# Kernel tuning notes

Hardware: AMD Instinct MI355X
Metric: run time of the kernel (lower is better)

The kernel has to match this reference:

```python
import jax, jax.numpy as jnp
import numpy as np

B, T, L, D = 2, 32, 64, 1024
H, WS, SH = 16, 8, 4
HD = D // H
EPS = 1e-6


def setup_inputs() -> dict:
    key = jax.random.key(0)
    ks = jax.random.split(key, 12)
    f = lambda i, shape, s=1.0: jax.random.normal(ks[i], shape, dtype=jnp.float32) * s
    return {
        'audio': f(0, (B, T, L, D)),
        'video': f(1, (B, T, L, D)),
        'image': f(2, (B, T, L, D)),
        'Wq': f(3, (3, D, D), 0.02), 'Wk': f(4, (3, D, D), 0.02),
        'Wv': f(5, (3, D, D), 0.02), 'Wp': f(6, (3, D, D), 0.02),
        'bq': jnp.zeros((3, D)), 'bk': jnp.zeros((3, D)),
        'bv': jnp.zeros((3, D)), 'bp': jnp.zeros((3, D)),
        'qn': jnp.ones((3, HD)), 'kn': jnp.ones((3, HD)),
        'rpb': f(7, (3, 2 * WS - 1, H), 0.02),
        'Wg1': f(8, (3 * D, 2 * D), 0.02), 'bg1': jnp.zeros((2 * D,)),
        'Wg2': f(9, (2 * D, 3), 0.02), 'bg2': jnp.zeros((3,)),
    }


def _rms(x, w):
    # OmniRMSNorm over last dim (head_dim)
    v = jnp.mean(x * x, axis=-1, keepdims=True)
    return w * (x * jax.lax.rsqrt(v + EPS))


def _wca(q_in, kv_in, Wq, bq, Wk, bk, Wv, bv, qn, kn, rpb, Wp, bp):
    """Shifted temporal-window cross attention. q_in, kv_in: [B,T,L,D]."""
    nw = T // WS
    S = WS * L  # tokens per window
    qr = jnp.roll(q_in, -SH, axis=1).reshape(B * nw, S, D)
    kr = jnp.roll(kv_in, -SH, axis=1).reshape(B * nw, S, D)
    q = (qr @ Wq + bq).reshape(B * nw, S, H, HD).transpose(0, 2, 1, 3)
    k = (kr @ Wk + bk).reshape(B * nw, S, H, HD).transpose(0, 2, 1, 3)
    v = (kr @ Wv + bv).reshape(B * nw, S, H, HD).transpose(0, 2, 1, 3)
    q = _rms(q, qn)
    k = _rms(k, kn)
    attn = jnp.einsum('bhqd,bhkd->bhqk', q, k) * (HD ** -0.5)
    # relative position bias over temporal coords within window: [H, WS, WS]
    coords = jnp.arange(WS)
    idx = coords[:, None] - coords[None, :] + WS - 1
    bias = rpb[idx].transpose(2, 0, 1)
    attn = attn.reshape(B * nw, H, WS, L, WS, L) + bias[None, :, :, None, :, None]
    attn = jax.nn.softmax(attn.reshape(B * nw, H, S, S), axis=-1)
    out = jnp.einsum('bhqk,bhkd->bhqd', attn, v)
    out = out.transpose(0, 2, 1, 3).reshape(B * nw, S, D) @ Wp + bp
    out = out.reshape(B, T, L, D)
    return jnp.roll(out, SH, axis=1)


def reference(audio, video, image, Wq, Wk, Wv, Wp, bq, bk, bv, bp,
              qn, kn, rpb, Wg1, bg1, Wg2, bg2):
    pairs = [(audio, video), (video, audio), (image, video)]
    feats = []
    for j, (qm, cm) in enumerate(pairs):
        o = _wca(qm, cm, Wq[j], bq[j], Wk[j], bk[j], Wv[j], bv[j],
                 qn[j], kn[j], rpb[j], Wp[j], bp[j])
        feats.append((qm + o).reshape(B, T * L, D))
    cat = jnp.concatenate(feats, axis=-1)                 # [B, TL, 3D]
    g = jax.nn.gelu(cat @ Wg1 + bg1, approximate=False) @ Wg2 + bg2
    gates = jax.nn.softmax(g, axis=-1)                    # [B, TL, 3]
    fused = sum(gates[..., m:m + 1] * feats[m] for m in range(3))
    return fused.reshape(B, T, L, D)
```

## Files before the change

### kernel.cpp

```cpp
#include <hip/hip_runtime.h>
#include <hip/hip_bf16.h>
#include <math.h>


typedef __bf16 bf16x8 __attribute__((ext_vector_type(8)));
typedef float f32x4 __attribute__((ext_vector_type(4)));

#define ELEM4M 4194304ull
#define ELEM1M 1048576ull

__device__ __forceinline__ float b2f(short s) {
    unsigned u = ((unsigned)(unsigned short)s) << 16;
    float f; __builtin_memcpy(&f, &u, 4); return f;
}
__device__ __forceinline__ short f2b(float f) {
    unsigned u; __builtin_memcpy(&u, &f, 4);
    u = (u + 0x7fffu + ((u >> 16) & 1u)) >> 16;
    return (short)u;
}

__global__ __launch_bounds__(256) void cast_roll_k(
    const float* __restrict__ a, const float* __restrict__ v,
    const float* __restrict__ im, short* __restrict__ dst)
{
    int z = blockIdx.y;
    const float* src = (z == 0) ? a : ((z == 1) ? v : im);
    int i = (blockIdx.x * 256 + threadIdx.x) * 4;
    int row = i >> 10, d = i & 1023;
    int b = row >> 11, tp = (row >> 6) & 31, l = row & 63;
    int srow = (b << 11) + (((tp + 4) & 31) << 6) + l;
    float4 val = *(const float4*)(src + (size_t)srow * 1024 + d);
    short4 o;
    o.x = f2b(val.x); o.y = f2b(val.y); o.z = f2b(val.z); o.w = f2b(val.w);
    *(short4*)(dst + (size_t)z * ELEM4M + i) = o;
}

__device__ __forceinline__ void transpose_body(const float* __restrict__ src,
                                               short* __restrict__ dst, int K, int N)
{
    __shared__ float tile[32][33];
    int x = blockIdx.x * 32 + threadIdx.x;
    int y0 = blockIdx.y * 32;
#pragma unroll
    for (int i = 0; i < 32; i += 8)
        tile[threadIdx.y + i][threadIdx.x] = src[(size_t)(y0 + threadIdx.y + i) * N + x];
    __syncthreads();
    int x2 = y0 + threadIdx.x;
    int y2 = blockIdx.x * 32 + threadIdx.y;
#pragma unroll
    for (int i = 0; i < 32; i += 8)
        dst[(size_t)(y2 + i) * K + x2] = f2b(tile[threadIdx.x][threadIdx.y + i]);
}

__global__ void transpose_qkvp_k(const float* Wq, const float* Wk, const float* Wv,
                                 const float* Wp, short* dst)
{
    int z = blockIdx.z;
    int g = z / 3, j = z - g * 3;
    const float* s4[4] = {Wq, Wk, Wv, Wp};
    transpose_body(s4[g] + (size_t)j * ELEM1M, dst + (size_t)z * ELEM1M, 1024, 1024);
}

__global__ void transpose_wg1_k(const float* Wg1, short* dst)
{
    transpose_body(Wg1, dst, 3072, 2048);
}

__global__ __launch_bounds__(256) void transpose_v_k(const short* __restrict__ V,
                                                     short* __restrict__ Vt)
{
    __shared__ short tile[64][65];
    int j = blockIdx.z;
    int c0 = blockIdx.x * 64, t0 = blockIdx.y * 64;
    const short* src = V + (size_t)j * ELEM4M;
    short* dst = Vt + (size_t)j * ELEM4M;
    int x = threadIdx.x & 63, y4 = threadIdx.x >> 6;
#pragma unroll
    for (int i = 0; i < 16; i++) {
        int row = y4 * 16 + i;
        tile[row][x] = src[(size_t)(t0 + row) * 1024 + c0 + x];
    }
    __syncthreads();
#pragma unroll
    for (int i = 0; i < 16; i++) {
        int row = y4 * 16 + i;
        dst[(size_t)(c0 + row) * 4096 + t0 + x] = tile[x][row];
    }
}

template<bool GELU, bool RES>
__device__ __forceinline__ void gemm_core(
    const short* __restrict__ A, const short* __restrict__ Wt,
    const float* __restrict__ bias, const short* __restrict__ Res,
    const float* __restrict__ nw, float nscale,
    short* __restrict__ C, int ldc, int colOff, int Ksz)
{
    __shared__ __align__(16) short As[128 * 32];
    __shared__ __align__(16) short Bs[128 * 32];
    const int tid = threadIdx.x;
    const int wave = tid >> 6, lane = tid & 63, quad = lane >> 4, l15 = lane & 15;
    const int wm = (wave & 1) * 64, wn = (wave >> 1) * 64;
    const int row0 = blockIdx.x * 128, col0 = blockIdx.y * 128;
    const int crow = lane >> 2, cseg = lane & 3;

    auto* As3 = (__attribute__((address_space(3))) short*)As;
    auto* Bs3 = (__attribute__((address_space(3))) short*)Bs;

    f32x4 acc[4][4];
#pragma unroll
    for (int i = 0; i < 4; i++)
#pragma unroll
        for (int jj = 0; jj < 4; jj++) acc[i][jj] = f32x4{0.f, 0.f, 0.f, 0.f};

    for (int k0 = 0; k0 < Ksz; k0 += 32) {
#pragma unroll
        for (int half = 0; half < 2; half++) {
            int chunk = wave + half * 4;
            const short* ga = A + (size_t)(row0 + chunk * 16 + crow) * Ksz + k0 + cseg * 8;
            const short* gb = Wt + (size_t)(col0 + chunk * 16 + crow) * Ksz + k0 + cseg * 8;
            __builtin_amdgcn_global_load_lds(
                (const __attribute__((address_space(1))) void*)ga,
                (__attribute__((address_space(3))) void*)(As3 + chunk * 512), 16, 0, 0);
            __builtin_amdgcn_global_load_lds(
                (const __attribute__((address_space(1))) void*)gb,
                (__attribute__((address_space(3))) void*)(Bs3 + chunk * 512), 16, 0, 0);
        }
        __syncthreads();
        bf16x8 af[4], bfr[4];
#pragma unroll
        for (int mi = 0; mi < 4; mi++)
            af[mi] = *(const bf16x8*)(As + (wm + mi * 16 + l15) * 32 + quad * 8);
#pragma unroll
        for (int ni = 0; ni < 4; ni++)
            bfr[ni] = *(const bf16x8*)(Bs + (wn + ni * 16 + l15) * 32 + quad * 8);
#pragma unroll
        for (int mi = 0; mi < 4; mi++)
#pragma unroll
            for (int ni = 0; ni < 4; ni++)
                acc[mi][ni] = __builtin_amdgcn_mfma_f32_16x16x32_bf16(
                    af[mi], bfr[ni], acc[mi][ni], 0, 0, 0);
        __syncthreads();
    }

    float bv4[4];
#pragma unroll
    for (int ni = 0; ni < 4; ni++) bv4[ni] = bias[col0 + wn + ni * 16 + l15];

    if (nw != nullptr) {
        float w4[4];
#pragma unroll
        for (int ni = 0; ni < 4; ni++) w4[ni] = nw[ni * 16 + l15];
#pragma unroll
        for (int mi = 0; mi < 4; mi++)
#pragma unroll
            for (int r = 0; r < 4; r++) {
                float v0 = acc[mi][0][r] + bv4[0];
                float v1 = acc[mi][1][r] + bv4[1];
                float v2 = acc[mi][2][r] + bv4[2];
                float v3 = acc[mi][3][r] + bv4[3];
                float ss = v0 * v0 + v1 * v1 + v2 * v2 + v3 * v3;
                ss += __shfl_xor(ss, 1); ss += __shfl_xor(ss, 2);
                ss += __shfl_xor(ss, 4); ss += __shfl_xor(ss, 8);
                float sc = rsqrtf(ss * (1.0f / 64.0f) + 1e-6f) * nscale;
                int row = row0 + wm + mi * 16 + quad * 4 + r;
                short* cp = C + (size_t)row * ldc + colOff + col0 + wn + l15;
                cp[0]  = f2b(v0 * sc * w4[0]);
                cp[16] = f2b(v1 * sc * w4[1]);
                cp[32] = f2b(v2 * sc * w4[2]);
                cp[48] = f2b(v3 * sc * w4[3]);
            }
    } else {
#pragma unroll
        for (int mi = 0; mi < 4; mi++)
#pragma unroll
            for (int ni = 0; ni < 4; ni++) {
                int col = col0 + wn + ni * 16 + l15;
#pragma unroll
                for (int r = 0; r < 4; r++) {
                    int row = row0 + wm + mi * 16 + quad * 4 + r;
                    float v = acc[mi][ni][r] + bv4[ni];
                    if (GELU) v = 0.5f * v * (1.0f + erff(v * 0.70710678118f));
                    if (RES)  v += b2f(Res[(size_t)row * 1024 + col]);
                    C[(size_t)row * ldc + colOff + col] = f2b(v);
                }
            }
    }
}

__global__ __launch_bounds__(256) void gemm_qkv_k(
    const short* r0, const short* r1, const short* r2,
    const short* Wt, const float* bq, const float* bk, const float* bv,
    const float* qn, const float* kn, short* qkv)
{
    int z = blockIdx.z;
    int g = z / 3, j = z - g * 3;
    const short* rolled[3] = {r0, r1, r2};
    const int kvmap[3] = {1, 0, 1};
    const short* A = (g == 0) ? rolled[j] : rolled[kvmap[j]];
    const float* bias = ((g == 0) ? bq : ((g == 1) ? bk : bv)) + j * 1024;
    const float* nw = (g == 0) ? (qn + j * 64) : ((g == 1) ? (kn + j * 64) : nullptr);
    float nscale = (g == 0) ? 0.125f : 1.0f;
    gemm_core<false, false>(A, Wt + (size_t)z * ELEM1M, bias, nullptr, nw, nscale,
                            qkv + (size_t)z * ELEM4M, 1024, 0, 1024);
}

__global__ __launch_bounds__(256) void gemm_out_k(
    const short* attnO, const short* Wt9, const float* bp,
    const short* r0, const short* r1, const short* r2, short* fcat)
{
    int j = blockIdx.z;
    const short* rolled[3] = {r0, r1, r2};
    gemm_core<false, true>(attnO + (size_t)j * ELEM4M, Wt9 + (size_t)j * ELEM1M,
                           bp + j * 1024, rolled[j], nullptr, 1.0f, fcat, 3072, j * 1024, 1024);
}

__global__ __launch_bounds__(256) void gemm_gate_k(
    const short* fcat, const short* Wg1t, const float* bg1, short* g1)
{
    gemm_core<true, false>(fcat, Wg1t, bg1, nullptr, nullptr, 1.0f, g1, 2048, 0, 3072);
}

__global__ __launch_bounds__(256, 2) void attn_k(
    const short* __restrict__ qkv, const short* __restrict__ Vt,
    const float* __restrict__ rpb, short* __restrict__ attnO)
{
    const int qhalf = blockIdx.x;
    const int win = blockIdx.y >> 4, h = blockIdx.y & 15;
    const int j = blockIdx.z;
    const int tid = threadIdx.x, wave = tid >> 6, lane = tid & 63;
    const int quad = lane >> 4, l15 = lane & 15;

    __shared__ __align__(16) short Ks[64 * 64];
    __shared__ __align__(16) short Vc[64 * 64];
    __shared__ __align__(16) short Ps[4][2][16 * 80];

    auto* Ks3 = (__attribute__((address_space(3))) short*)Ks;
    auto* Vc3 = (__attribute__((address_space(3))) short*)Vc;

    const int tq = qhalf * 4 + wave;
    const int qrow0 = win * 512 + tq * 64;
    const short* Qb = qkv + (size_t)j * ELEM4M + (size_t)qrow0 * 1024 + h * 64;
    const short* Kb = qkv + (size_t)(3 + j) * ELEM4M + (size_t)(win * 512) * 1024 + h * 64;
    const short* Vb = Vt + (size_t)j * ELEM4M + (size_t)(h * 64) * 4096 + win * 512;

    auto stage = [&](int ck) {
#pragma unroll
        for (int i = 0; i < 2; i++) {
            int s0 = (wave * 2 + i) * 64;
            int slot = s0 + lane;
            int r = slot >> 3, sw = ((slot & 7) ^ (r & 7)) * 8;
            const short* gk = Kb + (size_t)(ck * 64 + r) * 1024 + sw;
            const short* gv = Vb + (size_t)r * 4096 + ck * 64 + sw;
            __builtin_amdgcn_global_load_lds(
                (const __attribute__((address_space(1))) void*)gk,
                (__attribute__((address_space(3))) void*)(Ks3 + s0 * 8), 16, 0, 0);
            __builtin_amdgcn_global_load_lds(
                (const __attribute__((address_space(1))) void*)gv,
                (__attribute__((address_space(3))) void*)(Vc3 + s0 * 8), 16, 0, 0);
        }
    };

    bf16x8 qa[4][2];
#pragma unroll
    for (int qt = 0; qt < 4; qt++)
#pragma unroll
        for (int ks = 0; ks < 2; ks++)
            qa[qt][ks] = *(const bf16x8*)(Qb + (size_t)(qt * 16 + l15) * 1024
                                          + ks * 32 + quad * 8);

    f32x4 oacc[4][4];
#pragma unroll
    for (int qt = 0; qt < 4; qt++)
#pragma unroll
        for (int on = 0; on < 4; on++) oacc[qt][on] = f32x4{0.f, 0.f, 0.f, 0.f};
    float psum[4] = {0.f, 0.f, 0.f, 0.f};
    const float* rpbj = rpb + j * 240;

    stage(0);
    for (int ck = 0; ck < 8; ck++) {
        __syncthreads();
        bf16x8 kb[4][2], vb[4][2];
        const int swz = (l15 & 7);
#pragma unroll
        for (int t = 0; t < 4; t++)
#pragma unroll
            for (int ks = 0; ks < 2; ks++) {
                int row = t * 16 + l15;
                int off = row * 64 + (((ks * 4 + quad) ^ swz) * 8);
                kb[t][ks] = *(const bf16x8*)(Ks + off);
                vb[t][ks] = *(const bf16x8*)(Vc + off);
            }
        __syncthreads();
        if (ck < 7) stage(ck + 1);

        float bv = rpbj[(tq - ck + 7) * 16 + h];
#pragma unroll
        for (int qt = 0; qt < 4; qt++) {
            f32x4 sacc[4];
#pragma unroll
            for (int kn = 0; kn < 4; kn++) sacc[kn] = f32x4{0.f, 0.f, 0.f, 0.f};
#pragma unroll
            for (int ks = 0; ks < 2; ks++)
#pragma unroll
                for (int kn = 0; kn < 4; kn++)
                    sacc[kn] = __builtin_amdgcn_mfma_f32_16x16x32_bf16(
                        kb[kn][ks], qa[qt][ks], sacc[kn], 0, 0, 0);

            short* Pw = &Ps[wave][qt & 1][0];
            float ps = 0.f;
#pragma unroll
            for (int kn = 0; kn < 4; kn++) {
                float p0 = __expf(sacc[kn][0] + bv);
                float p1 = __expf(sacc[kn][1] + bv);
                float p2 = __expf(sacc[kn][2] + bv);
                float p3 = __expf(sacc[kn][3] + bv);
                ps += (p0 + p1) + (p2 + p3);
                short4 pk;
                pk.x = f2b(p0); pk.y = f2b(p1); pk.z = f2b(p2); pk.w = f2b(p3);
                *(short4*)(Pw + l15 * 80 + kn * 16 + quad * 4) = pk;
            }
            psum[qt] += ps;
#pragma unroll
            for (int ks = 0; ks < 2; ks++) {
                bf16x8 pa = *(const bf16x8*)(Pw + l15 * 80 + ks * 32 + quad * 8);
#pragma unroll
                for (int on = 0; on < 4; on++)
                    oacc[qt][on] = __builtin_amdgcn_mfma_f32_16x16x32_bf16(
                        pa, vb[on][ks], oacc[qt][on], 0, 0, 0);
            }
        }
    }

    short* Op = attnO + (size_t)j * ELEM4M;
#pragma unroll
    for (int qt = 0; qt < 4; qt++) {
        float s = psum[qt];
        s += __shfl_xor(s, 16); s += __shfl_xor(s, 32);
        float inv = 1.0f / s;
        float invr[4];
#pragma unroll
        for (int r = 0; r < 4; r++) invr[r] = __shfl(inv, quad * 4 + r);
#pragma unroll
        for (int on = 0; on < 4; on++) {
            int col = h * 64 + on * 16 + l15;
#pragma unroll
            for (int r = 0; r < 4; r++) {
                int row = qrow0 + qt * 16 + quad * 4 + r;
                Op[(size_t)row * 1024 + col] = f2b(oacc[qt][on][r] * invr[r]);
            }
        }
    }
}

__global__ __launch_bounds__(256) void fuse_k(
    const short* __restrict__ g1, const short* __restrict__ fcat,
    const float* __restrict__ Wg2, const float* __restrict__ bg2,
    float* __restrict__ out)
{
    int row = blockIdx.x, tid = threadIdx.x;
    const short* gp = g1 + (size_t)row * 2048;
    float a0 = 0.f, a1 = 0.f, a2 = 0.f;
    for (int k = tid; k < 2048; k += 256) {
        float gv = b2f(gp[k]);
        a0 += gv * Wg2[k * 3 + 0];
        a1 += gv * Wg2[k * 3 + 1];
        a2 += gv * Wg2[k * 3 + 2];
    }
#pragma unroll
    for (int off = 1; off < 64; off <<= 1) {
        a0 += __shfl_xor(a0, off); a1 += __shfl_xor(a1, off); a2 += __shfl_xor(a2, off);
    }
    __shared__ float part[4][3];
    int wave = tid >> 6, lane = tid & 63;
    if (lane == 0) { part[wave][0] = a0; part[wave][1] = a1; part[wave][2] = a2; }
    __syncthreads();
    float g0 = part[0][0] + part[1][0] + part[2][0] + part[3][0] + bg2[0];
    float gA = part[0][1] + part[1][1] + part[2][1] + part[3][1] + bg2[1];
    float gB = part[0][2] + part[1][2] + part[2][2] + part[3][2] + bg2[2];
    float mx = fmaxf(g0, fmaxf(gA, gB));
    float e0 = __expf(g0 - mx), e1 = __expf(gA - mx), e2 = __expf(gB - mx);
    float inv = 1.0f / (e0 + e1 + e2);
    e0 *= inv; e1 *= inv; e2 *= inv;

    int b = row >> 11, tp = (row >> 6) & 31, l = row & 63;
    size_t orow = (size_t)(b * 32 + ((tp + 4) & 31)) * 64 + l;
    const short* f0 = fcat + (size_t)row * 3072;
    float* op = out + orow * 1024;
    for (int c = tid; c < 1024; c += 256)
        op[c] = e0 * b2f(f0[c]) + e1 * b2f(f0[1024 + c]) + e2 * b2f(f0[2048 + c]);
}

extern "C" void kernel_launch(void* const* d_in, const int* in_sizes, int n_in,
                              void* d_out, int out_size, void* d_ws, size_t ws_size,
                              hipStream_t stream)
{
    const float* audio = (const float*)d_in[0];
    const float* video = (const float*)d_in[1];
    const float* image = (const float*)d_in[2];
    const float* Wq = (const float*)d_in[3];
    const float* Wk = (const float*)d_in[4];
    const float* Wv = (const float*)d_in[5];
    const float* Wp = (const float*)d_in[6];
    const float* bq = (const float*)d_in[7];
    const float* bk = (const float*)d_in[8];
    const float* bv = (const float*)d_in[9];
    const float* bp = (const float*)d_in[10];
    const float* qn = (const float*)d_in[11];
    const float* kn = (const float*)d_in[12];
    const float* rpb = (const float*)d_in[13];
    const float* Wg1 = (const float*)d_in[14];
    const float* bg1 = (const float*)d_in[15];
    const float* Wg2 = (const float*)d_in[16];
    const float* bg2 = (const float*)d_in[17];
    float* out = (float*)d_out;

    short* ws = (short*)d_ws;
    short* rolled = ws;
    short* Wt     = rolled + 3 * ELEM4M;
    short* Wg1t   = Wt + 12 * ELEM1M;
    short* qkv    = Wg1t + 6 * ELEM1M;
    short* attnO  = qkv + 9 * ELEM4M;
    short* fcat   = attnO + 3 * ELEM4M;
    short* VtBuf  = fcat;
    short* g1buf  = qkv;

    cast_roll_k<<<dim3(4096, 3), 256, 0, stream>>>(audio, video, image, rolled);
    transpose_qkvp_k<<<dim3(32, 32, 12), dim3(32, 8), 0, stream>>>(Wq, Wk, Wv, Wp, Wt);
    transpose_wg1_k<<<dim3(64, 96), dim3(32, 8), 0, stream>>>(Wg1, Wg1t);
    gemm_qkv_k<<<dim3(32, 8, 9), 256, 0, stream>>>(
        rolled, rolled + ELEM4M, rolled + 2 * ELEM4M, Wt, bq, bk, bv, qn, kn, qkv);
    transpose_v_k<<<dim3(16, 64, 3), 256, 0, stream>>>(qkv + 6 * ELEM4M, VtBuf);
    attn_k<<<dim3(2, 128, 3), 256, 0, stream>>>(qkv, VtBuf, rpb, attnO);
    gemm_out_k<<<dim3(32, 8, 3), 256, 0, stream>>>(
        attnO, Wt + 9 * ELEM1M, bp, rolled, rolled + ELEM4M, rolled + 2 * ELEM4M, fcat);
    gemm_gate_k<<<dim3(32, 16), 256, 0, stream>>>(fcat, Wg1t, bg1, g1buf);
    fuse_k<<<4096, 256, 0, stream>>>(g1buf, fcat, Wg2, bg2, out);
}
```

Baseline: 486.5 us.

## Double K-tile to 64 with XOR-swizzled LDS and prefetch overlapping MFMA

The GEMM core now stages 64-wide K tiles instead of 32, with an XOR swizzle on the LDS column chunk to avoid bank conflicts on fragment reads. Fragments are loaded into registers and the next tile's global-to-LDS load is issued before the MFMAs run, so memory traffic overlaps with compute. This halves the number of barriers per K but doubles LDS use and raises register pressure from holding two K-slices of fragments.

```diff
diff --git a/kernel.cpp b/kernel.cpp
--- a/kernel.cpp
+++ b/kernel.cpp
@@ -95,51 +95,64 @@
     const float* __restrict__ nw, float nscale,
     short* __restrict__ C, int ldc, int colOff, int Ksz)
 {
-    __shared__ __align__(16) short As[128 * 32];
-    __shared__ __align__(16) short Bs[128 * 32];
+    __shared__ __align__(16) short As[128 * 64];
+    __shared__ __align__(16) short Bs[128 * 64];
     const int tid = threadIdx.x;
     const int wave = tid >> 6, lane = tid & 63, quad = lane >> 4, l15 = lane & 15;
     const int wm = (wave & 1) * 64, wn = (wave >> 1) * 64;
     const int row0 = blockIdx.x * 128, col0 = blockIdx.y * 128;
-    const int crow = lane >> 2, cseg = lane & 3;
 
     auto* As3 = (__attribute__((address_space(3))) short*)As;
     auto* Bs3 = (__attribute__((address_space(3))) short*)Bs;
 
-    f32x4 acc[4][4];
-#pragma unroll
-    for (int i = 0; i < 4; i++)
-#pragma unroll
-        for (int jj = 0; jj < 4; jj++) acc[i][jj] = f32x4{0.f, 0.f, 0.f, 0.f};
-
-    for (int k0 = 0; k0 < Ksz; k0 += 32) {
-#pragma unroll
-        for (int half = 0; half < 2; half++) {
-            int chunk = wave + half * 4;
-            const short* ga = A + (size_t)(row0 + chunk * 16 + crow) * Ksz + k0 + cseg * 8;
-            const short* gb = Wt + (size_t)(col0 + chunk * 16 + crow) * Ksz + k0 + cseg * 8;
+    const int s_lane_r = ((wave * 64 + lane) >> 3);
+    auto stage = [&](int k0) {
+#pragma unroll
+        for (int i = 0; i < 4; i++) {
+            int s0 = i * 256 + wave * 64;
+            int slot = s0 + lane;
+            int r = slot >> 3, c = slot & 7;
+            int gc = (c ^ (r & 7)) * 8;
+            const short* ga = A + (size_t)(row0 + r) * Ksz + k0 + gc;
+            const short* gb = Wt + (size_t)(col0 + r) * Ksz + k0 + gc;
             __builtin_amdgcn_global_load_lds(
                 (const __attribute__((address_space(1))) void*)ga,
-                (__attribute__((address_space(3))) void*)(As3 + chunk * 512), 16, 0, 0);
+                (__attribute__((address_space(3))) void*)(As3 + s0 * 8), 16, 0, 0);
             __builtin_amdgcn_global_load_lds(
                 (const __attribute__((address_space(1))) void*)gb,
-                (__attribute__((address_space(3))) void*)(Bs3 + chunk * 512), 16, 0, 0);
+                (__attribute__((address_space(3))) void*)(Bs3 + s0 * 8), 16, 0, 0);
         }
+    };
+
+    f32x4 acc[4][4];
+#pragma unroll
+    for (int i = 0; i < 4; i++)
+#pragma unroll
+        for (int jj = 0; jj < 4; jj++) acc[i][jj] = f32x4{0.f, 0.f, 0.f, 0.f};
+
+    const int swz = l15 & 7;
+    stage(0);
+    for (int k0 = 0; k0 < Ksz; k0 += 64) {
         __syncthreads();
-        bf16x8 af[4], bfr[4];
+        bf16x8 af[4][2], bfr[4][2];
 #pragma unroll
         for (int mi = 0; mi < 4; mi++)
-            af[mi] = *(const bf16x8*)(As + (wm + mi * 16 + l15) * 32 + quad * 8);
-#pragma unroll
-        for (int ni = 0; ni < 4; ni++)
-            bfr[ni] = *(const bf16x8*)(Bs + (wn + ni * 16 + l15) * 32 + quad * 8);
-#pragma unroll
-        for (int mi = 0; mi < 4; mi++)
-#pragma unroll
-            for (int ni = 0; ni < 4; ni++)
-                acc[mi][ni] = __builtin_amdgcn_mfma_f32_16x16x32_bf16(
-                    af[mi], bfr[ni], acc[mi][ni], 0, 0, 0);
+#pragma unroll
+            for (int ks = 0; ks < 2; ks++) {
+                int coff = ((ks * 4 + quad) ^ swz) * 8;
+                af[mi][ks]  = *(const bf16x8*)(As + (wm + mi * 16 + l15) * 64 + coff);
+                bfr[mi][ks] = *(const bf16x8*)(Bs + (wn + mi * 16 + l15) * 64 + coff);
+            }
         __syncthreads();
+        if (k0 + 64 < Ksz) stage(k0 + 64);
+#pragma unroll
+        for (int ks = 0; ks < 2; ks++)
+#pragma unroll
+            for (int mi = 0; mi < 4; mi++)
+#pragma unroll
+                for (int ni = 0; ni < 4; ni++)
+                    acc[mi][ni] = __builtin_amdgcn_mfma_f32_16x16x32_bf16(
+                        af[mi][ks], bfr[ni][ks], acc[mi][ni], 0, 0, 0);
     }
 
     float bv4[4];
```

Result: faster. 432.1 us (-11.2%).
